# Kernel tuning notes

Measured on AMD Instinct MI355X. Metric: run time of the kernel, lower is better.

## Reference

```python
import jax, jax.numpy as jnp
import numpy as np
import math


def wn_linear(x, v, g, b):
    # PyTorch weight_norm with dim=0: W[i] = g[i] * v[i] / ||v[i]||
    w = g[:, None] * v / jnp.linalg.norm(v, axis=1, keepdims=True)  # [out, in]
    return x @ w.T + b


def setup_inputs() -> dict:
    key = jax.random.key(0)
    ks = jax.random.split(key, 11)
    B, QC, KC, C, H, W = 8, 384, 384, 512, 32, 32
    s = 0.02
    return {
        "q": jax.random.normal(ks[0], (B, QC, H, W), jnp.float32),
        "k": jax.random.normal(ks[1], (B, KC, H, W), jnp.float32),
        "Wq_v": jax.random.normal(ks[2], (C, QC), jnp.float32) * s,
        "Wq_g": jax.random.uniform(ks[3], (C,), jnp.float32, 0.5, 1.5),
        "bq": jax.random.normal(ks[4], (C,), jnp.float32) * s,
        "Wk_v": jax.random.normal(ks[5], (C, KC), jnp.float32) * s,
        "Wk_g": jax.random.uniform(ks[6], (C,), jnp.float32, 0.5, 1.5),
        "bk": jax.random.normal(ks[7], (C,), jnp.float32) * s,
        "Wv_v": jax.random.normal(ks[8], (C, KC), jnp.float32) * s,
        "Wv_g": jax.random.uniform(ks[9], (C,), jnp.float32, 0.5, 1.5),
        "bv": jax.random.normal(ks[10], (C,), jnp.float32) * s,
    }


def reference(q, k, Wq_v, Wq_g, bq, Wk_v, Wk_g, bk, Wv_v, Wv_g, bv):
    NB_HEAD = 8
    B, _, H, W = k.shape
    S = H * W
    C = Wq_v.shape[0]
    D = C // NB_HEAD  # head_dim

    qf = q.reshape(B, q.shape[1], S).transpose(0, 2, 1)  # [B,S,QC]
    kf = k.reshape(B, k.shape[1], S).transpose(0, 2, 1)  # [B,S,KC]

    def heads(x):  # [B,S,C] -> [B,NH,S,D]
        return x.reshape(B, S, NB_HEAD, D).transpose(0, 2, 1, 3)

    qh = heads(wn_linear(qf, Wq_v, Wq_g, bq))
    kh = heads(wn_linear(kf, Wk_v, Wk_g, bk))
    vh = heads(wn_linear(kf, Wv_v, Wv_g, bv))

    attn = jnp.einsum("bhqd,bhkd->bhqk", qh, kh) / math.sqrt(D)
    # mask = triu(ones,1).t() -> strictly lower triangular allowed (no diagonal)
    allowed = jnp.tril(jnp.ones((S, S), bool), -1)
    attn = jnp.where(allowed, attn, jnp.float32(-10000.0))
    attn = jax.nn.softmax(attn, axis=-1)
    # start_mask zeroes row 0 of the attention weights (post-softmax multiply)
    start_mask = (jnp.arange(S) > 0).astype(attn.dtype)[None, None, :, None]
    attn = attn * start_mask
    # dropout in eval mode -> identity

    out = jnp.einsum("bhqk,bhkd->bhqd", attn, vh)  # [B,NH,S,D]
    out = out.transpose(0, 2, 1, 3).reshape(B, H, W, C).transpose(0, 3, 1, 2)
    return out
```

## Files before the change

kernel.cpp:

```cpp
#include <hip/hip_runtime.h>
#include <hip/hip_bf16.h>

typedef __attribute__((ext_vector_type(8))) __bf16 bf16x8;
typedef __attribute__((ext_vector_type(4))) float f32x4;

__device__ __forceinline__ f32x4 mfma16(bf16x8 a, bf16x8 b, f32x4 c) {
    return __builtin_amdgcn_mfma_f32_16x16x32_bf16(a, b, c, 0, 0, 0);
}

__device__ __forceinline__ unsigned short f2bf(float x) {
    union { float f; unsigned int u; } cv; cv.f = x;
    unsigned int r = cv.u + 0x7FFFu + ((cv.u >> 16) & 1u);
    return (unsigned short)(r >> 16);
}

__device__ __forceinline__ unsigned pack2(float a, float b) {
    return (unsigned)f2bf(a) | ((unsigned)f2bf(b) << 16);
}

__device__ __forceinline__ unsigned pk2(float a, float b) {
    float2 f2; f2.x = a; f2.y = b;
    __hip_bfloat162 h = __float22bfloat162_rn(f2);
    return *(unsigned*)&h;
}

__device__ __forceinline__ float fast_exp2(float x) {
    float r;
    asm("v_exp_f32 %0, %1" : "=v"(r) : "v"(x));
    return r;
}

__device__ __forceinline__ void permswap32(unsigned &a, unsigned &b) {
    asm("v_permlane32_swap_b32 %0, %1" : "+v"(a), "+v"(b));
}
__device__ __forceinline__ void permswap16(unsigned &a, unsigned &b) {
    asm("v_permlane16_swap_b32 %0, %1" : "+v"(a), "+v"(b));
}

__device__ __forceinline__ void gload_lds16(const void* g, void* l) {
    __builtin_amdgcn_global_load_lds(
        (const __attribute__((address_space(1))) unsigned int*)g,
        (__attribute__((address_space(3))) unsigned int*)l, 16, 0, 0);
}

__global__ __launch_bounds__(256) void prep_kernel(
    const float* __restrict__ q, const float* __restrict__ k,
    const float* __restrict__ Wq_v, const float* __restrict__ Wq_g,
    const float* __restrict__ Wk_v, const float* __restrict__ Wk_g,
    const float* __restrict__ Wv_v, const float* __restrict__ Wv_g,
    unsigned short* __restrict__ qT, unsigned short* __restrict__ kT,
    unsigned short* __restrict__ Wn)
{
    __shared__ float tile[32][33];
    int z = blockIdx.z;
    int t = threadIdx.x;
    if (z == 16) {
        int w = t >> 6, lane = t & 63;
        int idx = (blockIdx.y * 32 + blockIdx.x) * 4 + w;
        int proj = idx >> 9, o = idx & 511;
        const float* v = (proj == 0 ? Wq_v : proj == 1 ? Wk_v : Wv_v) + (size_t)o * 384;
        const float* g = (proj == 0 ? Wq_g : proj == 1 ? Wk_g : Wv_g);
        float vals[6];
        float ss = 0.f;
#pragma unroll
        for (int i = 0; i < 6; ++i) { vals[i] = v[lane + i * 64]; ss += vals[i] * vals[i]; }
#pragma unroll
        for (int off = 1; off < 64; off <<= 1) ss += __shfl_xor(ss, off, 64);
        float scale = g[o] * rsqrtf(ss);
        unsigned short* dst = Wn + (size_t)proj * 512 * 384;
#pragma unroll
        for (int i = 0; i < 6; ++i) {
            int c = lane + i * 64;
            dst[((size_t)(c >> 5) * 512 + o) * 32 + (c & 31)] = f2bf(vals[i] * scale);
        }
        return;
    }
    int tx = t & 31, ty = t >> 5;
    const float* src = (z < 8 ? q : k) + (size_t)(z & 7) * 384 * 1024;
    unsigned short* dst = (z < 8 ? qT : kT) + (size_t)(z & 7) * 1024 * 384;
    int c0 = blockIdx.y * 32, s0 = blockIdx.x * 32;
#pragma unroll
    for (int j = 0; j < 4; ++j)
        tile[ty + j * 8][tx] = src[(size_t)(c0 + ty + j * 8) * 1024 + s0 + tx];
    __syncthreads();
    int cp = tx & 15;
    int chunk = c0 >> 5;
#pragma unroll
    for (int j = 0; j < 2; ++j) {
        int ss = ty + (tx >> 4) * 8 + j * 16;
        *(unsigned*)&dst[((size_t)chunk * 1024 + s0 + ss) * 32 + 2 * cp] =
            pk2(tile[2 * cp][ss], tile[2 * cp + 1][ss]);
    }
}

__global__ __launch_bounds__(256) void proj_gemm(
    const unsigned short* __restrict__ qT, const unsigned short* __restrict__ kT,
    const unsigned short* __restrict__ Wn,
    const float* __restrict__ bq, const float* __restrict__ bk, const float* __restrict__ bv,
    unsigned short* __restrict__ Qp, unsigned short* __restrict__ Kp,
    unsigned short* __restrict__ Vt)
{
    __shared__ __align__(16) unsigned short pool[4][128 * 32];
    int zb = blockIdx.z; int proj = zb >> 3, b = zb & 7;
    const unsigned short* A = (proj == 0 ? qT : kT) + (size_t)b * 1024 * 384;
    const unsigned short* Bw = Wn + (size_t)proj * 512 * 384;
    const float* bias = proj == 0 ? bq : (proj == 1 ? bk : bv);
    int m0 = blockIdx.x * 128, n0 = blockIdx.y * 128;
    int t = threadIdx.x, w = t >> 6, lane = t & 63;
    int fr = lane & 15, fq = lane >> 4;
    int wm = (w >> 1) * 64, wn = (w & 1) * 64;

    f32x4 acc[4][4];
#pragma unroll
    for (int i = 0; i < 4; ++i)
#pragma unroll
        for (int j = 0; j < 4; ++j) acc[i][j] = (f32x4){0.f, 0.f, 0.f, 0.f};

    auto stageAB = [&](int k0, int bufi) {
        int ch = k0 >> 5;
        const unsigned short* ab = A + ((size_t)ch * 1024 + m0) * 32 + w * 1024 + lane * 8;
        const unsigned short* bb = Bw + ((size_t)ch * 512 + n0) * 32 + w * 1024 + lane * 8;
        gload_lds16(ab, &pool[bufi][w * 1024]);
        gload_lds16(ab + 512, &pool[bufi][w * 1024 + 512]);
        gload_lds16(bb, &pool[2 + bufi][w * 1024]);
        gload_lds16(bb + 512, &pool[2 + bufi][w * 1024 + 512]);
    };

    stageAB(0, 0);
    for (int ks = 0; ks < 12; ++ks) {
        if (ks < 11) {
            stageAB((ks + 1) * 32, (ks + 1) & 1);
            asm volatile("s_waitcnt vmcnt(4)" ::: "memory");
        } else {
            asm volatile("s_waitcnt vmcnt(0)" ::: "memory");
        }
        __builtin_amdgcn_s_barrier();
        int bi = ks & 1;
        bf16x8 af[4], bfr[4];
#pragma unroll
        for (int i = 0; i < 4; ++i)
            af[i] = *(const bf16x8*)&pool[bi][(wm + i * 16 + fr) * 32 + fq * 8];
#pragma unroll
        for (int i = 0; i < 4; ++i)
            bfr[i] = *(const bf16x8*)&pool[2 + bi][(wn + i * 16 + fr) * 32 + fq * 8];
#pragma unroll
        for (int mi = 0; mi < 4; ++mi)
#pragma unroll
            for (int ni = 0; ni < 4; ++ni)
                acc[mi][ni] = mfma16(af[mi], bfr[ni], acc[mi][ni]);
        asm volatile("s_waitcnt lgkmcnt(0)" ::: "memory");
        __builtin_amdgcn_s_barrier();
    }

    if (proj == 2) {
#pragma unroll
        for (int mi = 0; mi < 4; ++mi)
#pragma unroll
            for (int ni = 0; ni < 4; ++ni) {
                int c = n0 + wn + ni * 16 + fr;
                int s0 = m0 + wm + mi * 16 + fq * 4;
                float bc = bias[c];
                unsigned lo = pack2(acc[mi][ni][0] + bc, acc[mi][ni][1] + bc);
                unsigned hi = pack2(acc[mi][ni][2] + bc, acc[mi][ni][3] + bc);
                uint2 u; u.x = lo; u.y = hi;
                *(uint2*)&Vt[(((size_t)b * 512 + c) * 1024 + s0)] = u;
            }
    } else {
        unsigned short* Out = (proj == 0 ? Qp : Kp) + (size_t)b * 1024 * 512;
        float vscale = (proj == 0) ? 0.18033688011112043f : 1.0f;
        const int STR = 72;
        unsigned short* scr = &pool[0][0] + w * 2304;
#pragma unroll
        for (int p = 0; p < 2; ++p) {
#pragma unroll
            for (int mh = 0; mh < 2; ++mh) {
                int mi = p * 2 + mh;
#pragma unroll
                for (int ni = 0; ni < 4; ++ni) {
                    int c = n0 + wn + ni * 16 + fr;
                    float bc = bias[c];
#pragma unroll
                    for (int r = 0; r < 4; ++r)
                        scr[(mh * 16 + fq * 4 + r) * STR + ni * 16 + fr] =
                            f2bf((acc[mi][ni][r] + bc) * vscale);
                }
            }
            asm volatile("s_waitcnt lgkmcnt(0)" ::: "memory");
            int sp = lane >> 1, ch = (lane & 1) * 32;
            int s = m0 + wm + p * 32 + sp;
#pragma unroll
            for (int kk = 0; kk < 4; ++kk) {
                bf16x8 v = *(const bf16x8*)&scr[sp * STR + ch + 8 * kk];
                *(bf16x8*)&Out[(size_t)s * 512 + n0 + wn + ch + 8 * kk] = v;
            }
            asm volatile("s_waitcnt lgkmcnt(0)" ::: "memory");
        }
    }
}

__global__ __launch_bounds__(256, 6) void attn_kernel(
    const unsigned short* __restrict__ Qp, const unsigned short* __restrict__ Kp,
    const unsigned short* __restrict__ Vt, float* __restrict__ out)
{
    __shared__ __align__(16) unsigned short Kl[64 * 64];
    __shared__ __align__(16) unsigned short Vl[64 * 64];
    int y = blockIdx.y;
    int qtile = y < 4 ? y : (y < 8 ? 19 - y : (y < 12 ? 15 - y : y - 4));
    int bh = blockIdx.x, b = bh >> 3, h = bh & 7;
    int tid = threadIdx.x, w = tid >> 6, lane = tid & 63;
    int fr = lane & 15, fq = lane >> 4;
    const unsigned short* Qb = Qp + ((size_t)b * 1024) * 512 + h * 64;
    const unsigned short* Kb = Kp + ((size_t)b * 1024) * 512 + h * 64;
    const unsigned short* VTb = Vt + ((size_t)b * 512 + h * 64) * 1024;
    int f3 = fr & 7;
    int sw = 8 * ((lane & 7) ^ (lane >> 3));

    union { unsigned u[4]; bf16x8 v; } ones;
#pragma unroll
    for (int i = 0; i < 4; ++i) ones.u[i] = 0x3F803F80u;

    auto stage = [&](int kt) {
        int kbase = kt * 64;
#pragma unroll
        for (int i = 0; i < 2; ++i) {
            int r0 = w * 16 + i * 8;
            gload_lds16(Kb + (size_t)(kbase + r0 + (lane >> 3)) * 512 + sw,
                        &Kl[r0 * 64]);
        }
#pragma unroll
        for (int i = 0; i < 2; ++i) {
            int d0 = w * 16 + i * 8;
            gload_lds16(VTb + (size_t)(d0 + (lane >> 3)) * 1024 + kbase + sw,
                        &Vl[d0 * 64]);
        }
    };

    int row0 = qtile * 64 + w * 16;
    int nt = qtile + 1;
    int qrow = row0 + fr;

    bf16x8 qf0 = *(const bf16x8*)(Qb + (size_t)(row0 + fr) * 512 + fq * 8);
    bf16x8 qf1 = *(const bf16x8*)(Qb + (size_t)(row0 + fr) * 512 + 32 + fq * 8);

    f32x4 Ot[4];
#pragma unroll
    for (int f = 0; f < 4; ++f) Ot[f] = (f32x4){0.f, 0.f, 0.f, 0.f};
    float M = -128.f, L = 0.f;

    for (int kt = 0; kt < nt; ++kt) {
        int kbase = kt * 64;
        stage(kt);
        asm volatile("s_waitcnt vmcnt(0)" ::: "memory");
        __builtin_amdgcn_s_barrier();

        f32x4 S[4];
#pragma unroll
        for (int kg = 0; kg < 4; ++kg) {
            bf16x8 k0 = *(const bf16x8*)&Kl[(kg * 16 + fr) * 64 + ((fq ^ f3) * 8)];
            bf16x8 k1 = *(const bf16x8*)&Kl[(kg * 16 + fr) * 64 + (((4 + fq) ^ f3) * 8)];
            S[kg] = mfma16(k0, qf0, (f32x4){0.f, 0.f, 0.f, 0.f});
            S[kg] = mfma16(k1, qf1, S[kg]);
        }

        float vmax = -3e38f;
#pragma unroll
        for (int kg = 0; kg < 4; ++kg)
#pragma unroll
            for (int r = 0; r < 4; ++r) {
                int key = kbase + kg * 16 + fq * 4 + r;
                float sv = (key < qrow) ? S[kg][r] : -3e38f;
                S[kg][r] = sv;
                vmax = fmaxf(vmax, sv);
            }
        vmax = fmaxf(vmax, __shfl_xor(vmax, 16, 64));
        vmax = fmaxf(vmax, __shfl_xor(vmax, 32, 64));
        if (__any(vmax > M + 8.f)) {
            float Mn = fmaxf(M, vmax);
            float al = fast_exp2(M - Mn);
            L *= al;
            M = Mn;
#pragma unroll
            for (int f = 0; f < 4; ++f) {
                Ot[f][0] *= al; Ot[f][1] *= al; Ot[f][2] *= al; Ot[f][3] *= al;
            }
        }
#pragma unroll
        for (int kg = 0; kg < 4; ++kg)
#pragma unroll
            for (int r = 0; r < 4; ++r)
                S[kg][r] = fast_exp2(S[kg][r] - M);

        bf16x8 pb[2];
#pragma unroll
        for (int m = 0; m < 2; ++m) {
            unsigned A0 = pk2(S[2 * m][0], S[2 * m][1]);
            unsigned A1 = pk2(S[2 * m][2], S[2 * m][3]);
            unsigned B0 = pk2(S[2 * m + 1][0], S[2 * m + 1][1]);
            unsigned B1 = pk2(S[2 * m + 1][2], S[2 * m + 1][3]);
            permswap32(A0, B0); permswap16(A0, B0);
            permswap32(A1, B1); permswap16(A1, B1);
            union { unsigned u[4]; bf16x8 v; } pu;
            pu.u[0] = A0; pu.u[1] = A1; pu.u[2] = B0; pu.u[3] = B1;
            pb[m] = pu.v;
        }

        f32x4 accS = (f32x4){0.f, 0.f, 0.f, 0.f};
        accS = mfma16(ones.v, pb[0], accS);
        accS = mfma16(ones.v, pb[1], accS);
        L += accS[0];

#pragma unroll
        for (int m = 0; m < 2; ++m)
#pragma unroll
            for (int f = 0; f < 4; ++f) {
                bf16x8 vf = *(const bf16x8*)&Vl[(f * 16 + fr) * 64 + (((4 * m + fq) ^ f3) * 8)];
                Ot[f] = mfma16(vf, pb[m], Ot[f]);
            }

        asm volatile("s_waitcnt lgkmcnt(0)" ::: "memory");
        __builtin_amdgcn_s_barrier();
    }

    float rcp = (L > 0.f) ? 1.f / L : 0.f;
    int q = row0 + fr;
#pragma unroll
    for (int f = 0; f < 4; ++f)
#pragma unroll
        for (int rr = 0; rr < 4; ++rr) {
            int d = f * 16 + fq * 4 + rr;
            out[((size_t)b * 512 + h * 64 + d) * 1024 + q] = Ot[f][rr] * rcp;
        }
}

extern "C" void kernel_launch(void* const* d_in, const int* in_sizes, int n_in,
                              void* d_out, int out_size, void* d_ws, size_t ws_size,
                              hipStream_t stream) {
    const float* q    = (const float*)d_in[0];
    const float* k    = (const float*)d_in[1];
    const float* Wq_v = (const float*)d_in[2];
    const float* Wq_g = (const float*)d_in[3];
    const float* bq   = (const float*)d_in[4];
    const float* Wk_v = (const float*)d_in[5];
    const float* Wk_g = (const float*)d_in[6];
    const float* bk   = (const float*)d_in[7];
    const float* Wv_v = (const float*)d_in[8];
    const float* Wv_g = (const float*)d_in[9];
    const float* bv   = (const float*)d_in[10];
    float* out = (float*)d_out;

    char* ws = (char*)d_ws;
    unsigned short* qT = (unsigned short*)(ws + 0);
    unsigned short* kT = (unsigned short*)(ws + 6291456);
    unsigned short* Wn = (unsigned short*)(ws + 12582912);
    unsigned short* Qp = (unsigned short*)(ws + 13762560);
    unsigned short* Kp = (unsigned short*)(ws + 22151168);
    unsigned short* Vt = (unsigned short*)(ws + 30539776);

    prep_kernel<<<dim3(32, 12, 17), dim3(256), 0, stream>>>(
        q, k, Wq_v, Wq_g, Wk_v, Wk_g, Wv_v, Wv_g, qT, kT, Wn);
    proj_gemm<<<dim3(8, 4, 24), dim3(256), 0, stream>>>(qT, kT, Wn, bq, bk, bv, Qp, Kp, Vt);
    attn_kernel<<<dim3(64, 16), dim3(256), 0, stream>>>(Qp, Kp, Vt, out);
}
```

Before: 53.60 us.

## Fuse q/k transpose and bf16 cast into projection GEMM A-tile loading

The prep kernel no longer transposes q/k into bf16 intermediate buffers. The projection GEMM now reads fp32 activations directly from the NCHW layout, converts them to bf16 in registers and writes them to LDS with an XOR swizzle. Register double-buffering replaces the async global-to-LDS loads. This removes a full write and read of the transposed activations, but the GEMM's global loads become strided scalar fp32 reads. Each A tile is also re-read and re-converted by every N-block.

```diff
diff --git a/kernel.cpp b/kernel.cpp
--- a/kernel.cpp
+++ b/kernel.cpp
@@ -44,57 +44,33 @@
 }
 
 __global__ __launch_bounds__(256) void prep_kernel(
-    const float* __restrict__ q, const float* __restrict__ k,
     const float* __restrict__ Wq_v, const float* __restrict__ Wq_g,
     const float* __restrict__ Wk_v, const float* __restrict__ Wk_g,
     const float* __restrict__ Wv_v, const float* __restrict__ Wv_g,
-    unsigned short* __restrict__ qT, unsigned short* __restrict__ kT,
     unsigned short* __restrict__ Wn)
 {
-    __shared__ float tile[32][33];
-    int z = blockIdx.z;
-    int t = threadIdx.x;
-    if (z == 16) {
-        int w = t >> 6, lane = t & 63;
-        int idx = (blockIdx.y * 32 + blockIdx.x) * 4 + w;
-        int proj = idx >> 9, o = idx & 511;
-        const float* v = (proj == 0 ? Wq_v : proj == 1 ? Wk_v : Wv_v) + (size_t)o * 384;
-        const float* g = (proj == 0 ? Wq_g : proj == 1 ? Wk_g : Wv_g);
-        float vals[6];
-        float ss = 0.f;
-#pragma unroll
-        for (int i = 0; i < 6; ++i) { vals[i] = v[lane + i * 64]; ss += vals[i] * vals[i]; }
-#pragma unroll
-        for (int off = 1; off < 64; off <<= 1) ss += __shfl_xor(ss, off, 64);
-        float scale = g[o] * rsqrtf(ss);
-        unsigned short* dst = Wn + (size_t)proj * 512 * 384;
-#pragma unroll
-        for (int i = 0; i < 6; ++i) {
-            int c = lane + i * 64;
-            dst[((size_t)(c >> 5) * 512 + o) * 32 + (c & 31)] = f2bf(vals[i] * scale);
-        }
-        return;
+    int t = threadIdx.x, w = t >> 6, lane = t & 63;
+    int idx = blockIdx.x * 4 + w;
+    int proj = idx >> 9, o = idx & 511;
+    const float* v = (proj == 0 ? Wq_v : proj == 1 ? Wk_v : Wv_v) + (size_t)o * 384;
+    const float* g = (proj == 0 ? Wq_g : proj == 1 ? Wk_g : Wv_g);
+    float vals[6];
+    float ss = 0.f;
+#pragma unroll
+    for (int i = 0; i < 6; ++i) { vals[i] = v[lane + i * 64]; ss += vals[i] * vals[i]; }
+#pragma unroll
+    for (int off = 1; off < 64; off <<= 1) ss += __shfl_xor(ss, off, 64);
+    float scale = g[o] * rsqrtf(ss);
+    unsigned short* dst = Wn + (size_t)proj * 512 * 384;
+#pragma unroll
+    for (int i = 0; i < 6; ++i) {
+        int c = lane + i * 64;
+        dst[((size_t)(c >> 5) * 512 + o) * 32 + (c & 31)] = f2bf(vals[i] * scale);
     }
-    int tx = t & 31, ty = t >> 5;
-    const float* src = (z < 8 ? q : k) + (size_t)(z & 7) * 384 * 1024;
-    unsigned short* dst = (z < 8 ? qT : kT) + (size_t)(z & 7) * 1024 * 384;
-    int c0 = blockIdx.y * 32, s0 = blockIdx.x * 32;
-#pragma unroll
-    for (int j = 0; j < 4; ++j)
-        tile[ty + j * 8][tx] = src[(size_t)(c0 + ty + j * 8) * 1024 + s0 + tx];
-    __syncthreads();
-    int cp = tx & 15;
-    int chunk = c0 >> 5;
-#pragma unroll
-    for (int j = 0; j < 2; ++j) {
-        int ss = ty + (tx >> 4) * 8 + j * 16;
-        *(unsigned*)&dst[((size_t)chunk * 1024 + s0 + ss) * 32 + 2 * cp] =
-            pk2(tile[2 * cp][ss], tile[2 * cp + 1][ss]);
-    }
 }
 
 __global__ __launch_bounds__(256) void proj_gemm(
-    const unsigned short* __restrict__ qT, const unsigned short* __restrict__ kT,
+    const float* __restrict__ qf, const float* __restrict__ kf,
     const unsigned short* __restrict__ Wn,
     const float* __restrict__ bq, const float* __restrict__ bk, const float* __restrict__ bv,
     unsigned short* __restrict__ Qp, unsigned short* __restrict__ Kp,
@@ -102,7 +78,7 @@
 {
     __shared__ __align__(16) unsigned short pool[4][128 * 32];
     int zb = blockIdx.z; int proj = zb >> 3, b = zb & 7;
-    const unsigned short* A = (proj == 0 ? qT : kT) + (size_t)b * 1024 * 384;
+    const float* Af = (proj == 0 ? qf : kf) + (size_t)b * 384 * 1024;
     const unsigned short* Bw = Wn + (size_t)proj * 512 * 384;
     const float* bias = proj == 0 ? bq : (proj == 1 ? bk : bv);
     int m0 = blockIdx.x * 128, n0 = blockIdx.y * 128;
@@ -110,36 +86,50 @@
     int fr = lane & 15, fq = lane >> 4;
     int wm = (w >> 1) * 64, wn = (w & 1) * 64;
 
+    int sLoc = w * 32 + (lane & 31);
+    int sg = m0 + sLoc;
+    int koBase = (lane >> 5) * 8;
+    int swzS = ((sLoc >> 3) & 3) << 3;
+
     f32x4 acc[4][4];
 #pragma unroll
     for (int i = 0; i < 4; ++i)
 #pragma unroll
         for (int j = 0; j < 4; ++j) acc[i][j] = (f32x4){0.f, 0.f, 0.f, 0.f};
 
-    auto stageAB = [&](int k0, int bufi) {
+    auto loadA = [&](int k0, float (&va)[16]) {
+#pragma unroll
+        for (int it = 0; it < 2; ++it)
+#pragma unroll
+            for (int j = 0; j < 8; ++j)
+                va[it * 8 + j] = Af[(size_t)(k0 + koBase + it * 16 + j) * 1024 + sg];
+    };
+    auto loadB = [&](int k0, uint4 (&vb)[2]) {
         int ch = k0 >> 5;
-        const unsigned short* ab = A + ((size_t)ch * 1024 + m0) * 32 + w * 1024 + lane * 8;
         const unsigned short* bb = Bw + ((size_t)ch * 512 + n0) * 32 + w * 1024 + lane * 8;
-        gload_lds16(ab, &pool[bufi][w * 1024]);
-        gload_lds16(ab + 512, &pool[bufi][w * 1024 + 512]);
-        gload_lds16(bb, &pool[2 + bufi][w * 1024]);
-        gload_lds16(bb + 512, &pool[2 + bufi][w * 1024 + 512]);
-    };
-
-    stageAB(0, 0);
-    for (int ks = 0; ks < 12; ++ks) {
-        if (ks < 11) {
-            stageAB((ks + 1) * 32, (ks + 1) & 1);
-            asm volatile("s_waitcnt vmcnt(4)" ::: "memory");
-        } else {
-            asm volatile("s_waitcnt vmcnt(0)" ::: "memory");
-        }
-        __builtin_amdgcn_s_barrier();
-        int bi = ks & 1;
+        vb[0] = *(const uint4*)bb;
+        vb[1] = *(const uint4*)(bb + 512);
+    };
+    auto writeAB = [&](float (&va)[16], uint4 (&vb)[2], int bufi) {
+#pragma unroll
+        for (int it = 0; it < 2; ++it) {
+            uint4 p;
+            p.x = pk2(va[it * 8 + 0], va[it * 8 + 1]);
+            p.y = pk2(va[it * 8 + 2], va[it * 8 + 3]);
+            p.z = pk2(va[it * 8 + 4], va[it * 8 + 5]);
+            p.w = pk2(va[it * 8 + 6], va[it * 8 + 7]);
+            *(uint4*)&pool[bufi][sLoc * 32 + ((koBase + it * 16) ^ swzS)] = p;
+        }
+        *(uint4*)&pool[2 + bufi][w * 1024 + lane * 8] = vb[0];
+        *(uint4*)&pool[2 + bufi][w * 1024 + lane * 8 + 512] = vb[1];
+    };
+    auto compute = [&](int bi) {
         bf16x8 af[4], bfr[4];
 #pragma unroll
-        for (int i = 0; i < 4; ++i)
-            af[i] = *(const bf16x8*)&pool[bi][(wm + i * 16 + fr) * 32 + fq * 8];
+        for (int i = 0; i < 4; ++i) {
+            int sA = wm + i * 16 + fr;
+            af[i] = *(const bf16x8*)&pool[bi][sA * 32 + ((fq * 8) ^ (((sA >> 3) & 3) << 3))];
+        }
 #pragma unroll
         for (int i = 0; i < 4; ++i)
             bfr[i] = *(const bf16x8*)&pool[2 + bi][(wn + i * 16 + fr) * 32 + fq * 8];
@@ -148,7 +138,27 @@
 #pragma unroll
             for (int ni = 0; ni < 4; ++ni)
                 acc[mi][ni] = mfma16(af[mi], bfr[ni], acc[mi][ni]);
+    };
+
+    float va0[16], va1[16];
+    uint4 vb0[2], vb1[2];
+    loadA(0, va0); loadB(0, vb0);
+#pragma unroll 1
+    for (int kp = 0; kp < 6; ++kp) {
+        int ks0 = 2 * kp;
+        loadA((ks0 + 1) * 32, va1); loadB((ks0 + 1) * 32, vb1);
+        writeAB(va0, vb0, 0);
         asm volatile("s_waitcnt lgkmcnt(0)" ::: "memory");
+        __builtin_amdgcn_sched_barrier(0);
+        __builtin_amdgcn_s_barrier();
+        compute(0);
+        __builtin_amdgcn_s_barrier();
+        if (kp < 5) { loadA((ks0 + 2) * 32, va0); loadB((ks0 + 2) * 32, vb0); }
+        writeAB(va1, vb1, 1);
+        asm volatile("s_waitcnt lgkmcnt(0)" ::: "memory");
+        __builtin_amdgcn_sched_barrier(0);
+        __builtin_amdgcn_s_barrier();
+        compute(1);
         __builtin_amdgcn_s_barrier();
     }
 
@@ -349,15 +359,13 @@
     float* out = (float*)d_out;
 
     char* ws = (char*)d_ws;
-    unsigned short* qT = (unsigned short*)(ws + 0);
-    unsigned short* kT = (unsigned short*)(ws + 6291456);
     unsigned short* Wn = (unsigned short*)(ws + 12582912);
     unsigned short* Qp = (unsigned short*)(ws + 13762560);
     unsigned short* Kp = (unsigned short*)(ws + 22151168);
     unsigned short* Vt = (unsigned short*)(ws + 30539776);
 
-    prep_kernel<<<dim3(32, 12, 17), dim3(256), 0, stream>>>(
-        q, k, Wq_v, Wq_g, Wk_v, Wk_g, Wv_v, Wv_g, qT, kT, Wn);
-    proj_gemm<<<dim3(8, 4, 24), dim3(256), 0, stream>>>(qT, kT, Wn, bq, bk, bv, Qp, Kp, Vt);
+    prep_kernel<<<dim3(384), dim3(256), 0, stream>>>(
+        Wq_v, Wq_g, Wk_v, Wk_g, Wv_v, Wv_g, Wn);
+    proj_gemm<<<dim3(8, 4, 24), dim3(256), 0, stream>>>(q, k, Wn, bq, bk, bv, Qp, Kp, Vt);
     attn_kernel<<<dim3(64, 16), dim3(256), 0, stream>>>(Qp, Kp, Vt, out);
 }
```

Measured after the change: 69.39 us. 29.5% more time.
